# Optimization experiments

Measured on AMD Instinct MI355X. Metric: run time of the kernel, lower is better.

The kernel has to match this reference:

```python
import jax, jax.numpy as jnp
import numpy as np

N_NODES = 50000
N_EDGES = 800000
DIM = 96
N_LAYERS = 3
N_GRAPHS = 128
OUT_DIM = 10


def setup_inputs() -> dict:
    key = jax.random.key(0)
    ks = jax.random.split(key, 9)
    s = 1.0 / np.sqrt(DIM)
    return {
        "x": jax.random.normal(ks[0], (N_NODES, DIM), dtype=jnp.float32),
        "edge_index": jax.random.randint(ks[1], (2, N_EDGES), 0, N_NODES, dtype=jnp.int32),
        "batch": jnp.sort(jax.random.randint(ks[2], (N_NODES,), 0, N_GRAPHS, dtype=jnp.int32)),
        "W1": jax.random.normal(ks[3], (N_LAYERS, DIM, DIM), dtype=jnp.float32) * s,
        "W2": jax.random.normal(ks[4], (N_LAYERS, DIM, DIM), dtype=jnp.float32) * s,
        "cw1": jax.random.normal(ks[5], (DIM, DIM), dtype=jnp.float32) * s,
        "cb1": jax.random.normal(ks[6], (DIM,), dtype=jnp.float32) * s,
        "cw2": jax.random.normal(ks[7], (DIM, OUT_DIM), dtype=jnp.float32) * s,
        "cb2": jax.random.normal(ks[8], (OUT_DIM,), dtype=jnp.float32) * s,
    }


def reference(x, edge_index, batch, W1, W2, cw1, cb1, cw2, cb2):
    src, dst = edge_index[0], edge_index[1]
    h = x
    for l in range(N_LAYERS):
        self_part = h @ W1[l]                       # [N, D]
        # transform at node level then gather per edge (same math as per-edge W2(x_j))
        msg = (h @ W2[l])[src]                      # [E, D]
        neighbor_part = jax.ops.segment_sum(msg, dst, num_segments=N_NODES)
        h = jax.nn.relu(self_part + neighbor_part)
    graph_emb = jax.ops.segment_sum(h, batch, num_segments=N_GRAPHS)  # [G, D]
    hidden = jax.nn.relu(graph_emb @ cw1 + cb1)
    return hidden @ cw2 + cb2                       # [G, OUT_DIM]
```

## Files before the change

kernel.cpp:

```cpp
#include <hip/hip_runtime.h>

#define N_NODES   50000
#define N_EDGES   800000
#define DIM       96
#define N_GRAPHS  128
#define OUT_DIM   10
#define NPAD      50048
#define ZROW      N_NODES
#define NBINS     391
#define P1_BLOCKS 128
#define EPB       (N_EDGES / P1_BLOCKS)
#define SLICECAP  48
#define CAP       64
#define LPAD      104

#define CAST_NB   ((N_NODES * 12 + 255) / 256)
#define CONV_NB   ((3 * DIM * 2 * DIM + 255) / 256)

typedef __attribute__((ext_vector_type(8))) short          short8;
typedef __attribute__((ext_vector_type(8))) unsigned short u16x8;
typedef __attribute__((ext_vector_type(4))) float          f32x4;
typedef __attribute__((ext_vector_type(2))) float          f32x2;

__device__ __forceinline__ float b2f(unsigned short u) {
    union { unsigned int i; float f; } v; v.i = ((unsigned int)u) << 16; return v.f;
}
__device__ __forceinline__ unsigned short f2b(float f) {
    union { float f; unsigned int i; } v; v.f = f;
    unsigned int u = v.i;
    return (unsigned short)((u + 0x7fffu + ((u >> 16) & 1u)) >> 16);
}

#if __has_builtin(__builtin_amdgcn_cvt_pk_f32_fp8) && __has_builtin(__builtin_amdgcn_cvt_pk_fp8_f32)
#define HW_FP8 1
#endif

__device__ __forceinline__ float d8s(unsigned int b) {
    const unsigned int t = b & 0x7fu;
    union { unsigned int i; float f; } v;
    v.i = ((b & 0x80u) << 24) | ((t << 20) + (120u << 23));
    float sub = (float)(int)t * 0.001953125f;
    if (b & 0x80u) sub = -sub;
    return (t < 8u) ? sub : v.f;
}
__device__ __forceinline__ unsigned int e8s(float f) {
    union { float f; unsigned int i; } v; v.f = f;
    const unsigned int u = v.i;
    const unsigned int s = (u >> 24) & 0x80u;
    const float af = fabsf(f);
    if (af < 0.015625f) {
        int mi = (int)(af * 512.f + 0.5f);
        return s | (unsigned int)(mi > 7 ? 7 : mi);
    }
    const unsigned int r = (u & 0x7fffffffu) + 0x0007ffffu + ((u >> 20) & 1u);
    const int ee = (int)(r >> 23) - 120;
    if (ee > 15) return s | 0x7eu;
    return s | ((unsigned int)ee << 3) | ((r >> 20) & 7u);
}

template<bool HI> __device__ __forceinline__ f32x2 dec_pk(unsigned int d) {
#ifdef HW_FP8
    return __builtin_amdgcn_cvt_pk_f32_fp8((int)d, HI);
#else
    const unsigned int w = HI ? (d >> 16) : (d & 0xffffu);
    f32x2 r; r[0] = d8s(w & 0xffu); r[1] = d8s(w >> 8);
    return r;
#endif
}
template<bool HI> __device__ __forceinline__ unsigned int enc_pk(float a, float b,
                                                                 unsigned int old) {
#ifdef HW_FP8
    return (unsigned int)__builtin_amdgcn_cvt_pk_fp8_f32(a, b, (int)old, HI);
#else
    const unsigned int p = e8s(a) | (e8s(b) << 8);
    return HI ? ((old & 0x0000ffffu) | (p << 16)) : ((old & 0xffff0000u) | p);
#endif
}

__global__ __launch_bounds__(256) void prep_pass1(
    const float* __restrict__ x,  const float* __restrict__ W1,
    const float* __restrict__ W2, const int* __restrict__ src,
    const int* __restrict__ dst,  unsigned short* __restrict__ harr,
    unsigned short* __restrict__ harrB,
    unsigned char* __restrict__ shA, unsigned char* __restrict__ shB,
    unsigned short* __restrict__ Bt, int* __restrict__ binned,
    int* __restrict__ cnt)
{
    __shared__ int cur[NBINS];
    const int b = blockIdx.x;
    const int t = threadIdx.x;

    if (b < P1_BLOCKS) {
        const int e0 = b * EPB;
        for (int i = t; i < NBINS; i += 256) cur[i] = 0;
        __syncthreads();
        for (int e = e0 + t; e < e0 + EPB; e += 256) {
            const int d   = dst[e];
            const int bin = d >> 7;
            const int pos = atomicAdd(&cur[bin], 1);
            if (pos < SLICECAP)
                binned[((size_t)bin * P1_BLOCKS + b) * SLICECAP + pos]
                    = ((d & 127) << 16) | src[e];
        }
        __syncthreads();
        for (int i = t; i < NBINS; i += 256)
            cnt[i * P1_BLOCKS + b] = min(cur[i], SLICECAP);
    } else if (b < P1_BLOCKS + CAST_NB) {
        const int tid = (b - P1_BLOCKS) * 256 + t;
        if (tid >= N_NODES * 12) return;
        const int node = tid / 12;
        const int c    = (tid - node * 12) * 8;
        const float4 v0 = *(const float4*)(x + (size_t)node * DIM + c);
        const float4 v1 = *(const float4*)(x + (size_t)node * DIM + c + 4);
        u16x8 o;
        o[0] = f2b(v0.x); o[1] = f2b(v0.y); o[2] = f2b(v0.z); o[3] = f2b(v0.w);
        o[4] = f2b(v1.x); o[5] = f2b(v1.y); o[6] = f2b(v1.z); o[7] = f2b(v1.w);
        *(u16x8*)(harr + (size_t)node * DIM + c) = o;
        unsigned int da = 0u, db = 0u;
        da = enc_pk<false>(v0.x * 0.25f, v0.y * 0.25f, da);
        da = enc_pk<true >(v0.z * 0.25f, v0.w * 0.25f, da);
        db = enc_pk<false>(v1.x * 0.25f, v1.y * 0.25f, db);
        db = enc_pk<true >(v1.z * 0.25f, v1.w * 0.25f, db);
        uint2 ob; ob.x = da; ob.y = db;
        *(uint2*)(shA + (size_t)node * 96 + c) = ob;
    } else if (b < P1_BLOCKS + CAST_NB + CONV_NB) {
        const int idx = (b - P1_BLOCKS - CAST_NB) * 256 + t;
        if (idx >= 3 * DIM * 2 * DIM) return;
        const int l   = idx / (DIM * 2 * DIM);
        const int rem = idx - l * (DIM * 2 * DIM);
        const int n   = rem / (2 * DIM);
        const int k   = rem - n * (2 * DIM);
        const float v = (k < DIM) ? W1[(size_t)l * DIM * DIM + k * DIM + n]
                                  : W2[(size_t)l * DIM * DIM + (k - DIM) * DIM + n];
        Bt[idx] = f2b(v);
    } else {
        if (t < 24) {
            u16x8 z;
#pragma unroll
            for (int i = 0; i < 8; i++) z[i] = 0;
            unsigned short* p = (t < 12) ? (harr  + (size_t)ZROW * DIM + t * 8)
                                         : (harrB + (size_t)ZROW * DIM + (t - 12) * 8);
            *(u16x8*)p = z;
        } else if (t < 48) {
            const int i = t - 24;
            uint2 z; z.x = 0u; z.y = 0u;
            unsigned char* p = (i < 12) ? (shA + (size_t)ZROW * 96 + i * 8)
                                        : (shB + (size_t)ZROW * 96 + (i - 12) * 8);
            *(uint2*)p = z;
        }
    }
}

__global__ __launch_bounds__(256) void pass2_scatter(const int* __restrict__ cnt,
                                                     const int* __restrict__ binned,
                                                     int* __restrict__ csrc,
                                                     int* __restrict__ deg)
{
    __shared__ int ncnt[128];
    const int bin = blockIdx.x;
    const int t   = threadIdx.x;
    const int n0  = bin << 7;

    if (t < 128) ncnt[t] = 0;
    __syncthreads();

    const int slice = t >> 1;
    const int par   = t & 1;
    const int c     = cnt[bin * P1_BLOCKS + slice];
    const int* __restrict__ bb = binned + ((size_t)bin * P1_BLOCKS + slice) * SLICECAP;

    for (int i = par; i < c; i += 2) {
        const int v    = bb[i];
        const int dlow = v >> 16;
        const int s    = v & 0xffff;
        const int pos  = atomicAdd(&ncnt[dlow], 1);
        if (pos < CAP) csrc[(size_t)(n0 + dlow) * CAP + pos] = s;
    }
    __syncthreads();

    if (t < 128 && n0 + t < N_NODES) {
        const int dn = min(ncnt[t], CAP);
        const int dp = (dn + 3) & ~3;
        int* __restrict__ bkt = csrc + (size_t)(n0 + t) * CAP;
        for (int p = dn; p < dp; p++) bkt[p] = ZROW;
        deg[n0 + t] = dp;
    }
}

#define LOAD4(x0,x1,x2,x3,base) do {                                        \
    const int4 sI = *(const int4*)(bkt + (base));                           \
    x0 = *(const uint4*)(hb + (size_t)sI.x * 96);                           \
    x1 = *(const uint4*)(hb + (size_t)sI.y * 96);                           \
    x2 = *(const uint4*)(hb + (size_t)sI.z * 96);                           \
    x3 = *(const uint4*)(hb + (size_t)sI.w * 96);                           \
} while (0)

#define ACCD(dw, b0) do {                                                   \
    const f32x2 lo_ = dec_pk<false>(dw);                                    \
    const f32x2 hi_ = dec_pk<true >(dw);                                    \
    a[(b0) + 0] += lo_[0]; a[(b0) + 1] += lo_[1];                           \
    a[(b0) + 2] += hi_[0]; a[(b0) + 3] += hi_[1];                           \
} while (0)
#define ACC1(vv) do { ACCD(vv.x, 0); ACCD(vv.y, 4); ACCD(vv.z, 8); ACCD(vv.w, 12); } while (0)
#define ACC4(x0,x1,x2,x3) do { ACC1(x0); ACC1(x1); ACC1(x2); ACC1(x3); } while (0)

__global__ __launch_bounds__(384) void gnn_layer(
    const unsigned short* __restrict__ harr, const int* __restrict__ deg,
    const int* __restrict__ csrc, const unsigned short* __restrict__ Btl,
    unsigned short* __restrict__ hout,
    const unsigned char* __restrict__ shIn, unsigned char* __restrict__ shOut)
{
    __shared__ unsigned short aggLds[64][LPAD];
    const int t       = threadIdx.x;
    const int rowBase = blockIdx.x * 64;

    const int lane = t & 63;
    const int w    = t >> 6;
    const int m    = lane & 15;
    const int q    = lane >> 4;

    short8 bfrag[6];
#pragma unroll
    for (int s = 0; s < 6; s++)
        bfrag[s] = *(const short8*)(Btl + (size_t)(w * 16 + m) * (2 * DIM) + s * 32 + q * 8);

    {
        const int r    = t / 6;
        const int sub  = t - r * 6;
        const int node = rowBase + r;
        const int off  = sub * 16;

        float a[16];
#pragma unroll
        for (int i = 0; i < 16; i++) a[i] = 0.f;

        if (node < N_NODES) {
            const int nb = deg[node] >> 2;
            const int* __restrict__ bkt = csrc + (size_t)node * CAP;
            const unsigned char* __restrict__ hb = shIn + off;

            uint4 va0, va1, va2, va3;
            uint4 wa0, wa1, wa2, wa3;

            if (nb > 0) {
                LOAD4(va0, va1, va2, va3, 0);
                int b = 1;
                for (; b + 1 < nb; b += 2) {
                    LOAD4(wa0, wa1, wa2, wa3, b * 4);
                    ACC4(va0, va1, va2, va3);
                    LOAD4(va0, va1, va2, va3, (b + 1) * 4);
                    ACC4(wa0, wa1, wa2, wa3);
                }
                if (b < nb) {
                    LOAD4(wa0, wa1, wa2, wa3, b * 4);
                    ACC4(va0, va1, va2, va3);
                    ACC4(wa0, wa1, wa2, wa3);
                } else {
                    ACC4(va0, va1, va2, va3);
                }
            }
        }

        u16x8 o0, o1;
#pragma unroll
        for (int i = 0; i < 8; i++) {
            o0[i] = f2b(a[i] * 4.f);
            o1[i] = f2b(a[i + 8] * 4.f);
        }
        *(u16x8*)(&aggLds[r][off])     = o0;
        *(u16x8*)(&aggLds[r][off + 8]) = o1;
    }
    __syncthreads();

    f32x4 accv[4];
#pragma unroll
    for (int r = 0; r < 4; r++) {
        const int rb = rowBase + r * 16;
        f32x4 acc = {0.f, 0.f, 0.f, 0.f};
        const unsigned short* ah = harr + (size_t)(rb + m) * DIM + q * 8;
#pragma unroll
        for (int s = 0; s < 3; s++) {
            const short8 af = *(const short8*)(ah + s * 32);
            acc = __builtin_amdgcn_mfma_f32_16x16x32_bf16(af, bfrag[s], acc, 0, 0, 0);
        }
#pragma unroll
        for (int s = 0; s < 3; s++) {
            const short8 af = *(const short8*)(&aggLds[r * 16 + m][s * 32 + q * 8]);
            acc = __builtin_amdgcn_mfma_f32_16x16x32_bf16(af, bfrag[s + 3], acc, 0, 0, 0);
        }
        accv[r] = acc;
    }
    __syncthreads();

#pragma unroll
    for (int r = 0; r < 4; r++)
#pragma unroll
        for (int i = 0; i < 4; i++)
            aggLds[r * 16 + q * 4 + i][w * 16 + m] = f2b(fmaxf(accv[r][i], 0.f));
    __syncthreads();

#pragma unroll
    for (int k = 0; k < 2; k++) {
        const int idx = t + k * 384;
        const int row = idx / 12;
        const int ch  = idx - row * 12;
        const int grow = rowBase + row;
        if (grow < N_NODES)
            *(u16x8*)(hout + (size_t)grow * DIM + ch * 8)
                = *(const u16x8*)(&aggLds[row][ch * 8]);
    }
    {
        const int row  = t / 6;
        const int ch   = t - row * 6;
        const int grow = rowBase + row;
        if (grow < N_NODES) {
            const u16x8 h0 = *(const u16x8*)(&aggLds[row][ch * 16]);
            const u16x8 h1 = *(const u16x8*)(&aggLds[row][ch * 16 + 8]);
            unsigned int d0 = 0u, d1 = 0u, d2 = 0u, d3 = 0u;
            d0 = enc_pk<false>(b2f(h0[0]) * 0.25f, b2f(h0[1]) * 0.25f, d0);
            d0 = enc_pk<true >(b2f(h0[2]) * 0.25f, b2f(h0[3]) * 0.25f, d0);
            d1 = enc_pk<false>(b2f(h0[4]) * 0.25f, b2f(h0[5]) * 0.25f, d1);
            d1 = enc_pk<true >(b2f(h0[6]) * 0.25f, b2f(h0[7]) * 0.25f, d1);
            d2 = enc_pk<false>(b2f(h1[0]) * 0.25f, b2f(h1[1]) * 0.25f, d2);
            d2 = enc_pk<true >(b2f(h1[2]) * 0.25f, b2f(h1[3]) * 0.25f, d2);
            d3 = enc_pk<false>(b2f(h1[4]) * 0.25f, b2f(h1[5]) * 0.25f, d3);
            d3 = enc_pk<true >(b2f(h1[6]) * 0.25f, b2f(h1[7]) * 0.25f, d3);
            uint4 ob; ob.x = d0; ob.y = d1; ob.z = d2; ob.w = d3;
            *(uint4*)(shOut + (size_t)grow * 96 + ch * 16) = ob;
        }
    }
}

__global__ __launch_bounds__(960) void pool_classify(
    const unsigned short* __restrict__ h, const int* __restrict__ batch,
    const float* __restrict__ cw1, const float* __restrict__ cb1,
    const float* __restrict__ cw2, const float* __restrict__ cb2,
    float* __restrict__ out)
{
    const int g = blockIdx.x;
    const int t = threadIdx.x;

    int lo = 0, hi = N_NODES;
    while (lo < hi) { int m = (lo + hi) >> 1; if (batch[m] < g) lo = m + 1; else hi = m; }
    const int start = lo;
    hi = N_NODES;
    while (lo < hi) { int m = (lo + hi) >> 1; if (batch[m] < g + 1) lo = m + 1; else hi = m; }
    const int end = lo;

    __shared__ float part[10][DIM];
    __shared__ float gr[DIM];
    __shared__ float hid[DIM];

    const int col = t % DIM;
    const int ty  = t / DIM;

    float s = 0.f;
    for (int n = start + ty; n < end; n += 10)
        s += b2f(h[(size_t)n * DIM + col]);
    part[ty][col] = s;
    __syncthreads();
    if (ty == 0) {
        float acc = 0.f;
#pragma unroll
        for (int p = 0; p < 10; p++) acc += part[p][col];
        gr[col] = acc;
    }
    __syncthreads();

    if (ty < 4) {
        float hsum = 0.f;
        const int k0 = ty * (DIM / 4);
#pragma unroll 4
        for (int k = k0; k < k0 + DIM / 4; k++)
            hsum += gr[k] * cw1[k * DIM + col];
        part[ty][col] = hsum;
    }
    __syncthreads();
    if (ty == 0)
        hid[col] = fmaxf(part[0][col] + part[1][col] + part[2][col] + part[3][col]
                         + cb1[col], 0.f);
    __syncthreads();

    if (t < OUT_DIM) {
        float o = cb2[t];
#pragma unroll 4
        for (int k = 0; k < DIM; k++) o += hid[k] * cw2[k * OUT_DIM + t];
        out[g * OUT_DIM + t] = o;
    }
}

extern "C" void kernel_launch(void* const* d_in, const int* in_sizes, int n_in,
                              void* d_out, int out_size, void* d_ws, size_t ws_size,
                              hipStream_t stream)
{
    const float* x     = (const float*)d_in[0];
    const int*   ei    = (const int*)  d_in[1];
    const int*   batch = (const int*)  d_in[2];
    const float* W1    = (const float*)d_in[3];
    const float* W2    = (const float*)d_in[4];
    const float* cw1   = (const float*)d_in[5];
    const float* cb1   = (const float*)d_in[6];
    const float* cw2   = (const float*)d_in[7];
    const float* cb2   = (const float*)d_in[8];
    float*       out   = (float*)d_out;

    const int* src = ei;
    const int* dst = ei + N_EDGES;

    unsigned short* bufA = (unsigned short*)d_ws;
    unsigned short* bufB = bufA + (size_t)NPAD * DIM;
    unsigned short* Bt   = bufB + (size_t)NPAD * DIM;
    int*   cnt    = (int*)(Bt + 3 * DIM * 2 * DIM);
    int*   binned = cnt + NBINS * P1_BLOCKS;
    int*   csrc   = binned + (size_t)NBINS * P1_BLOCKS * SLICECAP;
    int*   deg    = csrc + (size_t)N_NODES * CAP;
    unsigned char* shA = (unsigned char*)(deg + N_NODES);
    unsigned char* shB = shA + (size_t)(N_NODES + 1) * 96;

    prep_pass1<<<P1_BLOCKS + CAST_NB + CONV_NB + 1, 256, 0, stream>>>(
        x, W1, W2, src, dst, bufA, bufB, shA, shB, Bt, binned, cnt);
    pass2_scatter<<<NBINS, 256, 0, stream>>>(cnt, binned, csrc, deg);

    unsigned short* hin  = bufA;
    unsigned short* hout = bufB;
    unsigned char*  shin = shA;
    unsigned char*  shout = shB;
    for (int l = 0; l < 3; l++) {
        gnn_layer<<<NPAD / 64, 384, 0, stream>>>(hin, deg, csrc,
                                                 Bt + (size_t)l * DIM * 2 * DIM,
                                                 hout, shin, shout);
        unsigned short* tmp = hin; hin = hout; hout = tmp;
        unsigned char*  tms = shin; shin = shout; shout = tms;
    }

    pool_classify<<<N_GRAPHS, 960, 0, stream>>>(hin, batch, cw1, cb1, cw2, cb2, out);
}
```

Before: 249.8 us.

## Fuse graph pooling into last GNN layer via atomic segment sums

The last layer now sums its ReLU outputs per graph directly from the MFMA accumulators. It uses the sorted batch ids and float atomics into a zeroed graph-embedding buffer, so it no longer writes h and the fp8 shadow to memory. The pool_classify kernel is replaced by a small classify kernel that only runs the two dense layers. This removes one full write and read of the final node features and the binary searches over batch, at the cost of global atomics and a nondeterministic float summation order.

```diff
diff --git a/kernel.cpp b/kernel.cpp
--- a/kernel.cpp
+++ b/kernel.cpp
@@ -84,7 +84,7 @@
     unsigned short* __restrict__ harrB,
     unsigned char* __restrict__ shA, unsigned char* __restrict__ shB,
     unsigned short* __restrict__ Bt, int* __restrict__ binned,
-    int* __restrict__ cnt)
+    int* __restrict__ cnt, float* __restrict__ gr)
 {
     __shared__ int cur[NBINS];
     const int b = blockIdx.x;
@@ -148,6 +148,9 @@
                                         : (shB + (size_t)ZROW * 96 + (i - 12) * 8);
             *(uint2*)p = z;
         }
+        float4* g4 = (float4*)gr;
+#pragma unroll
+        for (int i = 0; i < 12; i++) g4[t * 12 + i] = make_float4(0.f, 0.f, 0.f, 0.f);
     }
 }
 
@@ -204,13 +207,16 @@
 #define ACC1(vv) do { ACCD(vv.x, 0); ACCD(vv.y, 4); ACCD(vv.z, 8); ACCD(vv.w, 12); } while (0)
 #define ACC4(x0,x1,x2,x3) do { ACC1(x0); ACC1(x1); ACC1(x2); ACC1(x3); } while (0)
 
+template<bool LAST>
 __global__ __launch_bounds__(384) void gnn_layer(
     const unsigned short* __restrict__ harr, const int* __restrict__ deg,
     const int* __restrict__ csrc, const unsigned short* __restrict__ Btl,
     unsigned short* __restrict__ hout,
-    const unsigned char* __restrict__ shIn, unsigned char* __restrict__ shOut)
+    const unsigned char* __restrict__ shIn, unsigned char* __restrict__ shOut,
+    const int* __restrict__ batch, float* __restrict__ gr)
 {
     __shared__ unsigned short aggLds[64][LPAD];
+    __shared__ int batchLds[64];
     const int t       = threadIdx.x;
     const int rowBase = blockIdx.x * 64;
 
@@ -218,6 +224,11 @@
     const int w    = t >> 6;
     const int m    = lane & 15;
     const int q    = lane >> 4;
+
+    if constexpr (LAST) {
+        if (t < 64)
+            batchLds[t] = (rowBase + t < N_NODES) ? batch[rowBase + t] : -1;
+    }
 
     short8 bfrag[6];
 #pragma unroll
@@ -290,49 +301,73 @@
         }
         accv[r] = acc;
     }
-    __syncthreads();
-
-#pragma unroll
-    for (int r = 0; r < 4; r++)
-#pragma unroll
-        for (int i = 0; i < 4; i++)
-            aggLds[r * 16 + q * 4 + i][w * 16 + m] = f2b(fmaxf(accv[r][i], 0.f));
-    __syncthreads();
-
-#pragma unroll
-    for (int k = 0; k < 2; k++) {
-        const int idx = t + k * 384;
-        const int row = idx / 12;
-        const int ch  = idx - row * 12;
-        const int grow = rowBase + row;
-        if (grow < N_NODES)
-            *(u16x8*)(hout + (size_t)grow * DIM + ch * 8)
-                = *(const u16x8*)(&aggLds[row][ch * 8]);
-    }
-    {
-        const int row  = t / 6;
-        const int ch   = t - row * 6;
-        const int grow = rowBase + row;
-        if (grow < N_NODES) {
-            const u16x8 h0 = *(const u16x8*)(&aggLds[row][ch * 16]);
-            const u16x8 h1 = *(const u16x8*)(&aggLds[row][ch * 16 + 8]);
-            unsigned int d0 = 0u, d1 = 0u, d2 = 0u, d3 = 0u;
-            d0 = enc_pk<false>(b2f(h0[0]) * 0.25f, b2f(h0[1]) * 0.25f, d0);
-            d0 = enc_pk<true >(b2f(h0[2]) * 0.25f, b2f(h0[3]) * 0.25f, d0);
-            d1 = enc_pk<false>(b2f(h0[4]) * 0.25f, b2f(h0[5]) * 0.25f, d1);
-            d1 = enc_pk<true >(b2f(h0[6]) * 0.25f, b2f(h0[7]) * 0.25f, d1);
-            d2 = enc_pk<false>(b2f(h1[0]) * 0.25f, b2f(h1[1]) * 0.25f, d2);
-            d2 = enc_pk<true >(b2f(h1[2]) * 0.25f, b2f(h1[3]) * 0.25f, d2);
-            d3 = enc_pk<false>(b2f(h1[4]) * 0.25f, b2f(h1[5]) * 0.25f, d3);
-            d3 = enc_pk<true >(b2f(h1[6]) * 0.25f, b2f(h1[7]) * 0.25f, d3);
-            uint4 ob; ob.x = d0; ob.y = d1; ob.z = d2; ob.w = d3;
-            *(uint4*)(shOut + (size_t)grow * 96 + ch * 16) = ob;
-        }
-    }
-}
-
-__global__ __launch_bounds__(960) void pool_classify(
-    const unsigned short* __restrict__ h, const int* __restrict__ batch,
+
+    if constexpr (LAST) {
+        const int col = w * 16 + m;
+        int   curg = -1;
+        float sum  = 0.f;
+#pragma unroll
+        for (int r = 0; r < 4; r++) {
+#pragma unroll
+            for (int i = 0; i < 4; i++) {
+                const int g = batchLds[r * 16 + q * 4 + i];
+                const float v = fmaxf(accv[r][i], 0.f);
+                if (g < 0) {
+                    if (curg >= 0) { atomicAdd(&gr[curg * DIM + col], sum); curg = -1; }
+                } else if (g != curg) {
+                    if (curg >= 0) atomicAdd(&gr[curg * DIM + col], sum);
+                    curg = g; sum = v;
+                } else {
+                    sum += v;
+                }
+            }
+        }
+        if (curg >= 0) atomicAdd(&gr[curg * DIM + col], sum);
+    } else {
+        __syncthreads();
+
+#pragma unroll
+        for (int r = 0; r < 4; r++)
+#pragma unroll
+            for (int i = 0; i < 4; i++)
+                aggLds[r * 16 + q * 4 + i][w * 16 + m] = f2b(fmaxf(accv[r][i], 0.f));
+        __syncthreads();
+
+#pragma unroll
+        for (int k = 0; k < 2; k++) {
+            const int idx = t + k * 384;
+            const int row = idx / 12;
+            const int ch  = idx - row * 12;
+            const int grow = rowBase + row;
+            if (grow < N_NODES)
+                *(u16x8*)(hout + (size_t)grow * DIM + ch * 8)
+                    = *(const u16x8*)(&aggLds[row][ch * 8]);
+        }
+        {
+            const int row  = t / 6;
+            const int ch   = t - row * 6;
+            const int grow = rowBase + row;
+            if (grow < N_NODES) {
+                const u16x8 h0 = *(const u16x8*)(&aggLds[row][ch * 16]);
+                const u16x8 h1 = *(const u16x8*)(&aggLds[row][ch * 16 + 8]);
+                unsigned int d0 = 0u, d1 = 0u, d2 = 0u, d3 = 0u;
+                d0 = enc_pk<false>(b2f(h0[0]) * 0.25f, b2f(h0[1]) * 0.25f, d0);
+                d0 = enc_pk<true >(b2f(h0[2]) * 0.25f, b2f(h0[3]) * 0.25f, d0);
+                d1 = enc_pk<false>(b2f(h0[4]) * 0.25f, b2f(h0[5]) * 0.25f, d1);
+                d1 = enc_pk<true >(b2f(h0[6]) * 0.25f, b2f(h0[7]) * 0.25f, d1);
+                d2 = enc_pk<false>(b2f(h1[0]) * 0.25f, b2f(h1[1]) * 0.25f, d2);
+                d2 = enc_pk<true >(b2f(h1[2]) * 0.25f, b2f(h1[3]) * 0.25f, d2);
+                d3 = enc_pk<false>(b2f(h1[4]) * 0.25f, b2f(h1[5]) * 0.25f, d3);
+                d3 = enc_pk<true >(b2f(h1[6]) * 0.25f, b2f(h1[7]) * 0.25f, d3);
+                uint4 ob; ob.x = d0; ob.y = d1; ob.z = d2; ob.w = d3;
+                *(uint4*)(shOut + (size_t)grow * 96 + ch * 16) = ob;
+            }
+        }
+    }
+}
+
+__global__ __launch_bounds__(128) void classify(
+    const float* __restrict__ gr,
     const float* __restrict__ cw1, const float* __restrict__ cb1,
     const float* __restrict__ cw2, const float* __restrict__ cb2,
     float* __restrict__ out)
@@ -340,50 +375,23 @@
     const int g = blockIdx.x;
     const int t = threadIdx.x;
 
-    int lo = 0, hi = N_NODES;
-    while (lo < hi) { int m = (lo + hi) >> 1; if (batch[m] < g) lo = m + 1; else hi = m; }
-    const int start = lo;
-    hi = N_NODES;
-    while (lo < hi) { int m = (lo + hi) >> 1; if (batch[m] < g + 1) lo = m + 1; else hi = m; }
-    const int end = lo;
-
-    __shared__ float part[10][DIM];
-    __shared__ float gr[DIM];
+    __shared__ float grs[DIM];
     __shared__ float hid[DIM];
 
-    const int col = t % DIM;
-    const int ty  = t / DIM;
-
-    float s = 0.f;
-    for (int n = start + ty; n < end; n += 10)
-        s += b2f(h[(size_t)n * DIM + col]);
-    part[ty][col] = s;
+    if (t < DIM) grs[t] = gr[g * DIM + t];
     __syncthreads();
-    if (ty == 0) {
-        float acc = 0.f;
-#pragma unroll
-        for (int p = 0; p < 10; p++) acc += part[p][col];
-        gr[col] = acc;
-    }
-    __syncthreads();
-
-    if (ty < 4) {
-        float hsum = 0.f;
-        const int k0 = ty * (DIM / 4);
-#pragma unroll 4
-        for (int k = k0; k < k0 + DIM / 4; k++)
-            hsum += gr[k] * cw1[k * DIM + col];
-        part[ty][col] = hsum;
-    }
-    __syncthreads();
-    if (ty == 0)
-        hid[col] = fmaxf(part[0][col] + part[1][col] + part[2][col] + part[3][col]
-                         + cb1[col], 0.f);
+
+    if (t < DIM) {
+        float hsum = cb1[t];
+#pragma unroll 8
+        for (int k = 0; k < DIM; k++) hsum += grs[k] * cw1[k * DIM + t];
+        hid[t] = fmaxf(hsum, 0.f);
+    }
     __syncthreads();
 
     if (t < OUT_DIM) {
         float o = cb2[t];
-#pragma unroll 4
+#pragma unroll 8
         for (int k = 0; k < DIM; k++) o += hid[k] * cw2[k * OUT_DIM + t];
         out[g * OUT_DIM + t] = o;
     }
@@ -416,22 +424,20 @@
     int*   deg    = csrc + (size_t)N_NODES * CAP;
     unsigned char* shA = (unsigned char*)(deg + N_NODES);
     unsigned char* shB = shA + (size_t)(N_NODES + 1) * 96;
+    float* gr = (float*)(shB + (size_t)(N_NODES + 1) * 96);
 
     prep_pass1<<<P1_BLOCKS + CAST_NB + CONV_NB + 1, 256, 0, stream>>>(
-        x, W1, W2, src, dst, bufA, bufB, shA, shB, Bt, binned, cnt);
+        x, W1, W2, src, dst, bufA, bufB, shA, shB, Bt, binned, cnt, gr);
     pass2_scatter<<<NBINS, 256, 0, stream>>>(cnt, binned, csrc, deg);
 
-    unsigned short* hin  = bufA;
-    unsigned short* hout = bufB;
-    unsigned char*  shin = shA;
-    unsigned char*  shout = shB;
-    for (int l = 0; l < 3; l++) {
-        gnn_layer<<<NPAD / 64, 384, 0, stream>>>(hin, deg, csrc,
-                                                 Bt + (size_t)l * DIM * 2 * DIM,
-                                                 hout, shin, shout);
-        unsigned short* tmp = hin; hin = hout; hout = tmp;
-        unsigned char*  tms = shin; shin = shout; shout = tms;
-    }
-
-    pool_classify<<<N_GRAPHS, 960, 0, stream>>>(hin, batch, cw1, cb1, cw2, cb2, out);
-}
+    gnn_layer<false><<<NPAD / 64, 384, 0, stream>>>(bufA, deg, csrc, Bt,
+                                                    bufB, shA, shB, batch, gr);
+    gnn_layer<false><<<NPAD / 64, 384, 0, stream>>>(bufB, deg, csrc,
+                                                    Bt + (size_t)DIM * 2 * DIM,
+                                                    bufA, shB, shA, batch, gr);
+    gnn_layer<true><<<NPAD / 64, 384, 0, stream>>>(bufA, deg, csrc,
+                                                   Bt + (size_t)2 * DIM * 2 * DIM,
+                                                   bufB, shA, shB, batch, gr);
+
+    classify<<<N_GRAPHS, 128, 0, stream>>>(gr, cw1, cb1, cw2, cb2, out);
+}
```

After: 237.1 us. -5.1%, faster.
